# Performance work log

Measured on AMD Instinct MI355X. Metric: run time of the kernel, lower is better.

Reference implementation:

```python
import jax, jax.numpy as jnp
import numpy as np

N = 50000   # total residue nodes across the batch of peptides
E = 800000  # total directed intra-peptide edges (avg degree 16)
D = 512


def _w(k, shape):
    fan_in = shape[0]
    return (jax.random.normal(k, shape, jnp.float32) / np.sqrt(fan_in)).astype(jnp.float32)


def setup_inputs() -> dict:
    key = jax.random.key(0)
    ks = jax.random.split(key, 12)
    return {
        "peptide_feature": jax.random.normal(ks[0], (N, D), jnp.float32),
        "edge_index": jax.random.randint(ks[1], (2, E), 0, N),
        # aanet_proj: 512 -> 1024 -> 1024 -> 512 -> 80 (ReLU between, none after last)
        "W1": _w(ks[2], (512, 1024)), "b1": jnp.zeros((1024,), jnp.float32),
        "W2": _w(ks[3], (1024, 1024)), "b2": jnp.zeros((1024,), jnp.float32),
        "W3": _w(ks[4], (1024, 512)), "b3": jnp.zeros((512,), jnp.float32),
        "W4": _w(ks[5], (512, 80)), "b4": jnp.zeros((80,), jnp.float32),
        # in_net: 80 -> 512
        "Win": _w(ks[6], (80, 512)), "bin_": jnp.zeros((512,), jnp.float32),
        # GIN conv MLP: 512 -> 512 -> 512 (eps = 0)
        "Wg1": _w(ks[7], (512, 512)), "bg1": jnp.zeros((512,), jnp.float32),
        "Wg2": _w(ks[8], (512, 512)), "bg2": jnp.zeros((512,), jnp.float32),
        # out_net: 512 -> 80
        "Wout": _w(ks[9], (512, 80)), "bout": jnp.zeros((80,), jnp.float32),
    }


def reference(peptide_feature, edge_index, W1, b1, W2, b2, W3, b3, W4, b4,
              Win, bin_, Wg1, bg1, Wg2, bg2, Wout, bout):
    relu = jax.nn.relu
    # aanet_proj
    h = relu(peptide_feature @ W1 + b1)
    h = relu(h @ W2 + b2)
    h = relu(h @ W3 + b3)
    peptide_feat = h @ W4 + b4                      # [N, 80]
    # in_net
    x = peptide_feat @ Win + bin_                   # [N, 512]
    # GIN message passing (sum aggregation, eps=0): per-sample loop in the
    # original is equivalent to one global pass since edges are sample-local.
    src, dst = edge_index[0], edge_index[1]
    agg = jax.ops.segment_sum(x[src], dst, num_segments=N)   # [N, 512]
    g = x + agg
    g = relu(g @ Wg1 + bg1) @ Wg2 + bg2             # GIN MLP
    # out_net
    peptide_mask = g @ Wout + bout                  # [N, 80]
    return peptide_mask, peptide_feat
```

## Files before the change

kernel.cpp:

```cpp
#include <hip/hip_runtime.h>
#include <stdint.h>


using bf16x8 = __attribute__((ext_vector_type(8))) short;
using f32x4  = __attribute__((ext_vector_type(4))) float;

__device__ inline unsigned short f2bf(float f) {
    union { float f; unsigned u; } v; v.f = f;
    unsigned u = v.u;
    u += 0x7FFFu + ((u >> 16) & 1u);
    return (unsigned short)(u >> 16);
}
__device__ inline float bf2f(unsigned u16) {
    return __uint_as_float(u16 << 16);
}

struct PreDescs {
    const float* W[8]; unsigned short* Wt[8];
    int K[8], M[8], Kp[8], ntx[8], start[8];
    int tEnd, cEnd, eEnd;
    const float* feat; unsigned short* featb; int nFeat;
    const int* ei; int E; int* cnt;
};

__global__ __launch_bounds__(256) void rg_preprocess(PreDescs d) {
    int b = blockIdx.x;
    int tid = threadIdx.x;
    if (b < d.tEnd) {
        __shared__ float t[32][33];
        int di = 0;
#pragma unroll
        for (int i = 1; i < 8; ++i) if (b >= d.start[i]) di = i;
        int local = b - d.start[di];
        int bx = local % d.ntx[di];
        int by = local / d.ntx[di];
        const float* W = d.W[di];
        unsigned short* Wt = d.Wt[di];
        int K = d.K[di], M = d.M[di], Kp = d.Kp[di];
        int mb = bx * 32, kb = by * 32;
        int tx = tid & 31, tg = tid >> 5;
#pragma unroll
        for (int p = 0; p < 4; ++p) {
            int r = tg + p * 8;
            int k = kb + r, m = mb + tx;
            t[r][tx] = (k < K && m < M) ? W[(size_t)k * M + m] : 0.f;
        }
        __syncthreads();
#pragma unroll
        for (int p = 0; p < 4; ++p) {
            int r = tg + p * 8;
            int mo = mb + r, ko = kb + tx;
            Wt[(size_t)mo * Kp + ko] = f2bf(t[tx][r]);
        }
    } else if (b < d.cEnd) {
        int i = ((b - d.tEnd) * 256 + tid) * 4;
        if (i + 3 < d.nFeat) {
            float4 v = *(const float4*)(d.feat + i);
            ushort4 o; o.x = f2bf(v.x); o.y = f2bf(v.y); o.z = f2bf(v.z); o.w = f2bf(v.w);
            *(ushort4*)(d.featb + i) = o;
        }
    } else {
        int e = (b - d.cEnd) * 256 + tid;
        if (e < d.E) atomicAdd(&d.cnt[d.ei[d.E + e]], 1);
    }
}

template <bool RELU, bool OUT_BF, bool OUT_F32, bool DEGB>
__global__ __launch_bounds__(256) void rg_gemm(
    const unsigned short* __restrict__ A, const unsigned short* __restrict__ Bt,
    const float* __restrict__ bias, const int* __restrict__ deg, int Mvalid,
    unsigned short* __restrict__ outB, float* __restrict__ outF,
    int Nrows, int Kp, int Mp, int gN, int MT)
{
    __shared__ __align__(16) unsigned short As[128 * 64];
    __shared__ __align__(16) unsigned short Bs[128 * 64];

    int bid = blockIdx.x;
    int xcd = bid & 7;
    int slot = bid >> 3;
    int c = slot % MT;
    int rsub = slot / MT;
    int rt = rsub * 8 + xcd;
    if (rt >= gN) return;
    const int rowBase = rt * 128;
    const int nBase   = c * 128;

    const int tid  = threadIdx.x;
    const int lane = tid & 63;
    const int w    = tid >> 6;
    const int wm   = w & 1, wn = w >> 1;

    f32x4 acc[4][4];
#pragma unroll
    for (int i = 0; i < 4; ++i)
#pragma unroll
        for (int j = 0; j < 4; ++j) acc[i][j] = (f32x4){0.f, 0.f, 0.f, 0.f};

    const int nkt = Kp >> 6;
    for (int kt = 0; kt < nkt; ++kt) {
        __syncthreads();
        const int k0 = kt * 64;
#pragma unroll
        for (int i = 0; i < 4; ++i) {
            int q   = i * 256 + tid;
            int r   = q >> 3;
            int cbg = (q & 7) ^ (r & 7);
            int gr  = rowBase + r; if (gr >= Nrows) gr = Nrows - 1;
            const unsigned short* gp = A + (size_t)gr * Kp + k0 + cbg * 8;
            __builtin_amdgcn_global_load_lds(
                (const __attribute__((address_space(1))) void*)gp,
                (__attribute__((address_space(3))) void*)(&As[q * 8]), 16, 0, 0);
        }
#pragma unroll
        for (int i = 0; i < 4; ++i) {
            int q   = i * 256 + tid;
            int r   = q >> 3;
            int cbg = (q & 7) ^ (r & 7);
            const unsigned short* gp = Bt + (size_t)(nBase + r) * Kp + k0 + cbg * 8;
            __builtin_amdgcn_global_load_lds(
                (const __attribute__((address_space(1))) void*)gp,
                (__attribute__((address_space(3))) void*)(&Bs[q * 8]), 16, 0, 0);
        }
        __syncthreads();
#pragma unroll
        for (int kk = 0; kk < 2; ++kk) {
            bf16x8 a[4], b[4];
            const int cb = kk * 4 + (lane >> 4);
#pragma unroll
            for (int i = 0; i < 4; ++i) {
                int r = wm * 64 + i * 16 + (lane & 15);
                a[i] = *(const bf16x8*)&As[(r * 8 + (cb ^ (r & 7))) * 8];
            }
#pragma unroll
            for (int j = 0; j < 4; ++j) {
                int r = wn * 64 + j * 16 + (lane & 15);
                b[j] = *(const bf16x8*)&Bs[(r * 8 + (cb ^ (r & 7))) * 8];
            }
#pragma unroll
            for (int i = 0; i < 4; ++i)
#pragma unroll
                for (int j = 0; j < 4; ++j)
                    acc[i][j] = __builtin_amdgcn_mfma_f32_16x16x32_bf16(b[j], a[i], acc[i][j], 0, 0, 0);
        }
    }

    const int quad = lane >> 4;
#pragma unroll
    for (int i = 0; i < 4; ++i) {
        int row = rowBase + wm * 64 + i * 16 + (lane & 15);
        if (row >= Nrows) continue;
        float sc = 1.f;
        if (DEGB) sc = 1.f + (float)deg[row];
#pragma unroll
        for (int j = 0; j < 4; ++j) {
            int colb = nBase + wn * 64 + j * 16 + quad * 4;
            float4 bv = (colb < Mvalid) ? *(const float4*)(bias + colb)
                                        : (float4){0.f, 0.f, 0.f, 0.f};
            float v0 = acc[i][j][0] + sc * bv.x;
            float v1 = acc[i][j][1] + sc * bv.y;
            float v2 = acc[i][j][2] + sc * bv.z;
            float v3 = acc[i][j][3] + sc * bv.w;
            if (RELU) {
                v0 = v0 > 0.f ? v0 : 0.f; v1 = v1 > 0.f ? v1 : 0.f;
                v2 = v2 > 0.f ? v2 : 0.f; v3 = v3 > 0.f ? v3 : 0.f;
            }
            if (OUT_BF) {
                ushort4 o; o.x = f2bf(v0); o.y = f2bf(v1); o.z = f2bf(v2); o.w = f2bf(v3);
                *(ushort4*)(outB + (size_t)row * Mp + colb) = o;
            }
            if (OUT_F32) {
                if (colb < Mvalid)
                    *(float4*)(outF + (size_t)row * Mvalid + colb) = (float4){v0, v1, v2, v3};
            }
        }
    }
}

__global__ void rg_scan_block(const int* __restrict__ cnt, int* __restrict__ scanned,
                              int* __restrict__ bsums, int Nn) {
    __shared__ int sd[1024];
    int tid = threadIdx.x;
    int i = blockIdx.x * 1024 + tid;
    int v = (i < Nn) ? cnt[i] : 0;
    sd[tid] = v;
    __syncthreads();
    for (int off = 1; off < 1024; off <<= 1) {
        int t = (tid >= off) ? sd[tid - off] : 0;
        __syncthreads();
        sd[tid] += t;
        __syncthreads();
    }
    if (i < Nn) scanned[i] = sd[tid];
    if (tid == 1023) bsums[blockIdx.x] = sd[1023];
}

__global__ void rg_scan_sums(int* __restrict__ b, int nb) {
    if (threadIdx.x == 0) {
        int acc = 0;
        for (int i = 0; i < nb; ++i) { int t = b[i]; b[i] = acc; acc += t; }
    }
}

__global__ void rg_scan_add(const int* __restrict__ scanned, const int* __restrict__ bsums,
                            const int* __restrict__ cnt, int* __restrict__ rowptr,
                            int* __restrict__ cursor, int Nn, int E) {
    int i = blockIdx.x * 1024 + threadIdx.x;
    if (i < Nn) {
        int ex = scanned[i] - cnt[i] + bsums[blockIdx.x];
        rowptr[i] = ex; cursor[i] = ex;
    }
    if (i == 0) rowptr[Nn] = E;
}

__global__ void rg_scatter_edges(const int* __restrict__ ei, int E,
                                 int* __restrict__ cursor, int* __restrict__ cols) {
    int e = blockIdx.x * 256 + threadIdx.x;
    if (e < E) {
        int d = ei[E + e];
        int p = atomicAdd(&cursor[d], 1);
        cols[p] = ei[e];
    }
}

__global__ __launch_bounds__(256) void rg_agg80(
    const unsigned short* __restrict__ pf, const int* __restrict__ rowptr,
    const int* __restrict__ cols, unsigned short* __restrict__ s, int Nn)
{
    int node = blockIdx.x * 4 + (threadIdx.x >> 6);
    if (node >= Nn) return;
    int lane = threadIdx.x & 63;
    const unsigned* xp = (const unsigned*)pf;
    size_t off = (size_t)node * 64 + lane;
    unsigned u = xp[off];
    float a0 = bf2f(u & 0xffffu), a1 = bf2f(u >> 16);
    int beg = rowptr[node], end = rowptr[node + 1];
    for (int e = beg; e < end; ++e) {
        int src = cols[e];
        unsigned v = xp[(size_t)src * 64 + lane];
        a0 += bf2f(v & 0xffffu); a1 += bf2f(v >> 16);
    }
    unsigned o = (unsigned)f2bf(a0) | ((unsigned)f2bf(a1) << 16);
    ((unsigned*)s)[off] = o;
}

extern "C" void kernel_launch(void* const* d_in, const int* in_sizes, int n_in,
                              void* d_out, int out_size, void* d_ws, size_t ws_size,
                              hipStream_t stream)
{
    const float* feat = (const float*)d_in[0];
    const int*   ei   = (const int*)d_in[1];
    const float* W1 = (const float*)d_in[2];  const float* b1 = (const float*)d_in[3];
    const float* W2 = (const float*)d_in[4];  const float* b2 = (const float*)d_in[5];
    const float* W3 = (const float*)d_in[6];  const float* b3 = (const float*)d_in[7];
    const float* W4 = (const float*)d_in[8];  const float* b4 = (const float*)d_in[9];
    const float* Wi = (const float*)d_in[10]; const float* bi = (const float*)d_in[11];
    const float* Wg1 = (const float*)d_in[12]; const float* bg1 = (const float*)d_in[13];
    const float* Wg2 = (const float*)d_in[14]; const float* bg2 = (const float*)d_in[15];
    const float* Wo = (const float*)d_in[16]; const float* bo = (const float*)d_in[17];

    const int N = in_sizes[0] / 512;
    const int E = in_sizes[1] / 2;

    char* ws = (char*)d_ws;
    size_t o = 0;
    auto alloc = [&](size_t bytes) { char* p = ws + o; o += (bytes + 255) & ~(size_t)255; return p; };
    unsigned short* bufA = (unsigned short*)alloc((size_t)N * 1024 * 2);
    unsigned short* bufB = (unsigned short*)alloc((size_t)N * 1024 * 2);
    unsigned short* bufC = (unsigned short*)alloc((size_t)N * 512 * 2);
    unsigned short* W1t = (unsigned short*)alloc((size_t)1024 * 512 * 2);
    unsigned short* W2t = (unsigned short*)alloc((size_t)1024 * 1024 * 2);
    unsigned short* W3t = (unsigned short*)alloc((size_t)512 * 1024 * 2);
    unsigned short* W4t = (unsigned short*)alloc((size_t)128 * 512 * 2);
    unsigned short* Wit = (unsigned short*)alloc((size_t)512 * 128 * 2);
    unsigned short* Wg1t = (unsigned short*)alloc((size_t)512 * 512 * 2);
    unsigned short* Wg2t = (unsigned short*)alloc((size_t)512 * 512 * 2);
    unsigned short* Wot = (unsigned short*)alloc((size_t)128 * 512 * 2);
    int* cnt    = (int*)alloc((size_t)N * 4);
    int* rowptr = (int*)alloc((size_t)(N + 1) * 4);
    int* cursor = (int*)alloc((size_t)N * 4);
    int* cols   = (int*)alloc((size_t)E * 4);
    int* bsums  = (int*)alloc(256);

    float* out_mask = (float*)d_out;
    float* out_feat = (float*)d_out + (size_t)N * 80;

    hipMemsetAsync(cnt, 0, (size_t)N * 4, stream);
    {
        PreDescs d;
        const float* Ws[8]  = {W1, W2, W3, W4, Wi, Wg1, Wg2, Wo};
        unsigned short* Ts[8] = {W1t, W2t, W3t, W4t, Wit, Wg1t, Wg2t, Wot};
        int Ks[8]  = {512, 1024, 1024, 512, 80, 512, 512, 512};
        int Ms[8]  = {1024, 1024, 512, 80, 512, 512, 512, 80};
        int Kps[8] = {512, 1024, 1024, 512, 128, 512, 512, 512};
        int Mps[8] = {1024, 1024, 512, 128, 512, 512, 512, 128};
        int st = 0;
        for (int i = 0; i < 8; ++i) {
            d.W[i] = Ws[i]; d.Wt[i] = Ts[i];
            d.K[i] = Ks[i]; d.M[i] = Ms[i]; d.Kp[i] = Kps[i];
            d.ntx[i] = Mps[i] / 32;
            d.start[i] = st;
            st += (Mps[i] / 32) * (Kps[i] / 32);
        }
        d.tEnd = st;
        d.cEnd = st + (N * 512) / 1024;
        d.eEnd = d.cEnd + (E + 255) / 256;
        d.feat = feat; d.featb = bufC; d.nFeat = N * 512;
        d.ei = ei; d.E = E; d.cnt = cnt;
        rg_preprocess<<<d.eEnd, 256, 0, stream>>>(d);
    }

    int* scanned = cols;
    const int nb = (N + 1023) / 1024;
    rg_scan_block<<<nb, 1024, 0, stream>>>(cnt, scanned, bsums, N);
    rg_scan_sums<<<1, 64, 0, stream>>>(bsums, nb);
    rg_scan_add<<<nb, 1024, 0, stream>>>(scanned, bsums, cnt, rowptr, cursor, N, E);
    rg_scatter_edges<<<(E + 255) / 256, 256, 0, stream>>>(ei, E, cursor, cols);

    const int gN = (N + 127) / 128;
    const int rg8 = ((gN + 7) / 8) * 8;
    auto grid = [&](int MT) { return dim3(rg8 * MT); };

    rg_gemm<true, true, false, false><<<grid(8), 256, 0, stream>>>(bufC, W1t, b1, nullptr, 1024, bufA, nullptr, N, 512, 1024, gN, 8);
    rg_gemm<true, true, false, false><<<grid(8), 256, 0, stream>>>(bufA, W2t, b2, nullptr, 1024, bufB, nullptr, N, 1024, 1024, gN, 8);
    rg_gemm<true, true, false, false><<<grid(4), 256, 0, stream>>>(bufB, W3t, b3, nullptr, 512, bufC, nullptr, N, 1024, 512, gN, 4);
    rg_gemm<false, true, true, false><<<grid(1), 256, 0, stream>>>(bufC, W4t, b4, nullptr, 80, bufA, out_feat, N, 512, 128, gN, 1);

    rg_agg80<<<(N + 3) / 4, 256, 0, stream>>>(bufA, rowptr, cols, bufC, N);

    rg_gemm<false, true, false, true><<<grid(4), 256, 0, stream>>>(bufC, Wit, bi, cnt, 512, bufA, nullptr, N, 128, 512, gN, 4);
    rg_gemm<true, true, false, false><<<grid(4), 256, 0, stream>>>(bufA, Wg1t, bg1, nullptr, 512, bufB, nullptr, N, 512, 512, gN, 4);
    rg_gemm<false, true, false, false><<<grid(4), 256, 0, stream>>>(bufB, Wg2t, bg2, nullptr, 512, bufC, nullptr, N, 512, 512, gN, 4);
    rg_gemm<false, false, true, false><<<grid(1), 256, 0, stream>>>(bufC, Wot, bo, nullptr, 80, nullptr, out_mask, N, 512, 128, gN, 1);
}
```

Measured before the change: 846.5 us.

## Pad activation buffers, template GEMM column tiles, parallelize scan, unroll gather

Activation buffers are padded to a multiple of 128 rows so the GEMM A-tile loads can drop the per-row clamp. The column-tile count MT becomes a template parameter, so the slot division and modulo compile to constants. The block-sum scan now uses a warp shuffle scan instead of a single serial thread. The edge aggregation loop is unrolled by 8 to keep more gather loads in flight. Padded rows of the first GEMM input (featb in bufC) are never written, so those rows compute on garbage; only the outputs of valid rows are stored.

```diff
diff --git a/kernel.cpp b/kernel.cpp
--- a/kernel.cpp
+++ b/kernel.cpp
@@ -65,12 +65,12 @@
     }
 }
 
-template <bool RELU, bool OUT_BF, bool OUT_F32, bool DEGB>
+template <bool RELU, bool OUT_BF, bool OUT_F32, bool DEGB, int MT>
 __global__ __launch_bounds__(256) void rg_gemm(
     const unsigned short* __restrict__ A, const unsigned short* __restrict__ Bt,
     const float* __restrict__ bias, const int* __restrict__ deg, int Mvalid,
     unsigned short* __restrict__ outB, float* __restrict__ outF,
-    int Nrows, int Kp, int Mp, int gN, int MT)
+    int Nrows, int Kp, int Mp, int gN)
 {
     __shared__ __align__(16) unsigned short As[128 * 64];
     __shared__ __align__(16) unsigned short Bs[128 * 64];
@@ -105,8 +105,7 @@
             int q   = i * 256 + tid;
             int r   = q >> 3;
             int cbg = (q & 7) ^ (r & 7);
-            int gr  = rowBase + r; if (gr >= Nrows) gr = Nrows - 1;
-            const unsigned short* gp = A + (size_t)gr * Kp + k0 + cbg * 8;
+            const unsigned short* gp = A + (size_t)(rowBase + r) * Kp + k0 + cbg * 8;
             __builtin_amdgcn_global_load_lds(
                 (const __attribute__((address_space(1))) void*)gp,
                 (__attribute__((address_space(3))) void*)(&As[q * 8]), 16, 0, 0);
@@ -195,9 +194,19 @@
 }
 
 __global__ void rg_scan_sums(int* __restrict__ b, int nb) {
-    if (threadIdx.x == 0) {
-        int acc = 0;
-        for (int i = 0; i < nb; ++i) { int t = b[i]; b[i] = acc; acc += t; }
+    int tid = threadIdx.x;
+    int carry = 0;
+    for (int base = 0; base < nb; base += 64) {
+        int i = base + tid;
+        int v = (i < nb) ? b[i] : 0;
+        int incl = v;
+#pragma unroll
+        for (int off = 1; off < 64; off <<= 1) {
+            int t = __shfl_up(incl, off, 64);
+            if (tid >= off) incl += t;
+        }
+        if (i < nb) b[i] = carry + incl - v;
+        carry += __shfl(incl, 63, 64);
     }
 }
 
@@ -234,9 +243,16 @@
     unsigned u = xp[off];
     float a0 = bf2f(u & 0xffffu), a1 = bf2f(u >> 16);
     int beg = rowptr[node], end = rowptr[node + 1];
-    for (int e = beg; e < end; ++e) {
-        int src = cols[e];
-        unsigned v = xp[(size_t)src * 64 + lane];
+    int e = beg;
+    for (; e + 8 <= end; e += 8) {
+        unsigned v[8];
+#pragma unroll
+        for (int t = 0; t < 8; ++t) v[t] = xp[(size_t)cols[e + t] * 64 + lane];
+#pragma unroll
+        for (int t = 0; t < 8; ++t) { a0 += bf2f(v[t] & 0xffffu); a1 += bf2f(v[t] >> 16); }
+    }
+    for (; e < end; ++e) {
+        unsigned v = xp[(size_t)cols[e] * 64 + lane];
         a0 += bf2f(v & 0xffffu); a1 += bf2f(v >> 16);
     }
     unsigned o = (unsigned)f2bf(a0) | ((unsigned)f2bf(a1) << 16);
@@ -260,13 +276,15 @@
 
     const int N = in_sizes[0] / 512;
     const int E = in_sizes[1] / 2;
+    const int gN = (N + 127) / 128;
+    const int Npad = gN * 128;
 
     char* ws = (char*)d_ws;
     size_t o = 0;
     auto alloc = [&](size_t bytes) { char* p = ws + o; o += (bytes + 255) & ~(size_t)255; return p; };
-    unsigned short* bufA = (unsigned short*)alloc((size_t)N * 1024 * 2);
-    unsigned short* bufB = (unsigned short*)alloc((size_t)N * 1024 * 2);
-    unsigned short* bufC = (unsigned short*)alloc((size_t)N * 512 * 2);
+    unsigned short* bufA = (unsigned short*)alloc((size_t)Npad * 1024 * 2);
+    unsigned short* bufB = (unsigned short*)alloc((size_t)Npad * 1024 * 2);
+    unsigned short* bufC = (unsigned short*)alloc((size_t)Npad * 512 * 2);
     unsigned short* W1t = (unsigned short*)alloc((size_t)1024 * 512 * 2);
     unsigned short* W2t = (unsigned short*)alloc((size_t)1024 * 1024 * 2);
     unsigned short* W3t = (unsigned short*)alloc((size_t)512 * 1024 * 2);
@@ -316,19 +334,18 @@
     rg_scan_add<<<nb, 1024, 0, stream>>>(scanned, bsums, cnt, rowptr, cursor, N, E);
     rg_scatter_edges<<<(E + 255) / 256, 256, 0, stream>>>(ei, E, cursor, cols);
 
-    const int gN = (N + 127) / 128;
     const int rg8 = ((gN + 7) / 8) * 8;
     auto grid = [&](int MT) { return dim3(rg8 * MT); };
 
-    rg_gemm<true, true, false, false><<<grid(8), 256, 0, stream>>>(bufC, W1t, b1, nullptr, 1024, bufA, nullptr, N, 512, 1024, gN, 8);
-    rg_gemm<true, true, false, false><<<grid(8), 256, 0, stream>>>(bufA, W2t, b2, nullptr, 1024, bufB, nullptr, N, 1024, 1024, gN, 8);
-    rg_gemm<true, true, false, false><<<grid(4), 256, 0, stream>>>(bufB, W3t, b3, nullptr, 512, bufC, nullptr, N, 1024, 512, gN, 4);
-    rg_gemm<false, true, true, false><<<grid(1), 256, 0, stream>>>(bufC, W4t, b4, nullptr, 80, bufA, out_feat, N, 512, 128, gN, 1);
+    rg_gemm<true, true, false, false, 8><<<grid(8), 256, 0, stream>>>(bufC, W1t, b1, nullptr, 1024, bufA, nullptr, N, 512, 1024, gN);
+    rg_gemm<true, true, false, false, 8><<<grid(8), 256, 0, stream>>>(bufA, W2t, b2, nullptr, 1024, bufB, nullptr, N, 1024, 1024, gN);
+    rg_gemm<true, true, false, false, 4><<<grid(4), 256, 0, stream>>>(bufB, W3t, b3, nullptr, 512, bufC, nullptr, N, 1024, 512, gN);
+    rg_gemm<false, true, true, false, 1><<<grid(1), 256, 0, stream>>>(bufC, W4t, b4, nullptr, 80, bufA, out_feat, N, 512, 128, gN);
 
     rg_agg80<<<(N + 3) / 4, 256, 0, stream>>>(bufA, rowptr, cols, bufC, N);
 
-    rg_gemm<false, true, false, true><<<grid(4), 256, 0, stream>>>(bufC, Wit, bi, cnt, 512, bufA, nullptr, N, 128, 512, gN, 4);
-    rg_gemm<true, true, false, false><<<grid(4), 256, 0, stream>>>(bufA, Wg1t, bg1, nullptr, 512, bufB, nullptr, N, 512, 512, gN, 4);
-    rg_gemm<false, true, false, false><<<grid(4), 256, 0, stream>>>(bufB, Wg2t, bg2, nullptr, 512, bufC, nullptr, N, 512, 512, gN, 4);
-    rg_gemm<false, false, true, false><<<grid(1), 256, 0, stream>>>(bufC, Wot, bo, nullptr, 80, nullptr, out_mask, N, 512, 128, gN, 1);
-}
+    rg_gemm<false, true, false, true, 4><<<grid(4), 256, 0, stream>>>(bufC, Wit, bi, cnt, 512, bufA, nullptr, N, 128, 512, gN);
+    rg_gemm<true, true, false, false, 4><<<grid(4), 256, 0, stream>>>(bufA, Wg1t, bg1, nullptr, 512, bufB, nullptr, N, 512, 512, gN);
+    rg_gemm<false, true, false, false, 4><<<grid(4), 256, 0, stream>>>(bufB, Wg2t, bg2, nullptr, 512, bufC, nullptr, N, 512, 512, gN);
+    rg_gemm<false, false, true, false, 1><<<grid(1), 256, 0, stream>>>(bufC, Wot, bo, nullptr, 80, nullptr, out_mask, N, 512, 128, gN);
+}
```

Result: faster. 816.0 us (-3.6%).
